# Optimization experiments

Measured on AMD Instinct MI355X. Metric: run time of the kernel, lower is better.

Reference implementation:

```python
import jax, jax.numpy as jnp
import numpy as np

EMB = 128   # embedding_dim
ND = 128    # node_dim
B = 64      # graphs in batch
NN = 500    # n_nodes per graph
N = B * NN  # total nodes = 32000
E = 256000  # edges per edge set
M = 20      # history length in input_


def _lin_params(key, out_dim, in_dim, bias=True):
    k1, k2 = jax.random.split(key)
    s = 1.0 / np.sqrt(in_dim)
    w = jax.random.uniform(k1, (out_dim, in_dim), jnp.float32, -s, s)
    if bias:
        b = jax.random.uniform(k2, (out_dim,), jnp.float32, -s, s)
        return w, b
    return w


def setup_inputs() -> dict:
    key = jax.random.key(0)
    ks = jax.random.split(key, 40)
    inp = {}
    inp["state_"] = jax.random.normal(ks[0], (B, ND), jnp.float32)
    inp["input_"] = jax.random.normal(ks[1], (B, M, EMB), jnp.float32)
    inp["x"] = jax.random.normal(ks[2], (N, EMB), jnp.float32)
    inp["e_n"] = jax.random.randint(ks[3], (2, E), 0, N)
    inp["e_r0"] = jax.random.randint(ks[4], (2, E), 0, N)
    inp["e_r1"] = jax.random.randint(ks[5], (2, E), 0, N)
    inp["n_nodes"] = NN
    # GRU-like params
    inp["win"] = _lin_params(ks[6], ND, EMB, bias=False)
    inp["wz"], inp["bz"] = _lin_params(ks[7], ND, 2 * ND)
    inp["wr"], inp["br"] = _lin_params(ks[8], ND, 2 * ND)
    inp["wh"], inp["bh"] = _lin_params(ks[9], ND, 2 * ND)
    # GAT params: lin (out,in)+bias, attn (out, 2*out)+bias
    inp["g0_lw"], inp["g0_lb"] = _lin_params(ks[10], ND, EMB)
    inp["g0_aw"], inp["g0_ab"] = _lin_params(ks[11], ND, 2 * ND)
    inp["g1_lw"], inp["g1_lb"] = _lin_params(ks[12], ND, ND)
    inp["g1_aw"], inp["g1_ab"] = _lin_params(ks[13], ND, 2 * ND)
    inp["g2_lw"], inp["g2_lb"] = _lin_params(ks[14], ND, ND)
    inp["g2_aw"], inp["g2_ab"] = _lin_params(ks[15], ND, 2 * ND)
    inp["gn_lw"], inp["gn_lb"] = _lin_params(ks[16], ND, ND)
    inp["gn_aw"], inp["gn_ab"] = _lin_params(ks[17], ND, 2 * ND)
    # heads
    inp["pw"], inp["pb"] = _lin_params(ks[18], 1, ND)
    inp["mw"], inp["mb"] = _lin_params(ks[19], 1, ND)
    inp["sw"], inp["sb"] = _lin_params(ks[20], 1, ND)
    return inp


def gat_conv(x, ei, lw, lb, aw, ab, slope=0.2):
    """PyG GATConv variant: lin -> per-edge attn(cat(x_i,x_j)) -> leaky_relu ->
    per-dst segment softmax (per channel) -> scatter-add of x_j*alpha."""
    n = x.shape[0]
    sl = jnp.arange(n)
    src = jnp.concatenate([ei[0], sl])   # j (source)
    dst = jnp.concatenate([ei[1], sl])   # i (target; softmax + aggregation index)
    h = x @ lw.T + lb                    # [N, ND]
    hi = h[dst]                          # x_i  [E', ND]
    hj = h[src]                          # x_j  [E', ND]
    a = jnp.concatenate([hi, hj], axis=-1) @ aw.T + ab
    a = jax.nn.leaky_relu(a, slope)
    amax = jax.ops.segment_max(a, dst, num_segments=n)
    e = jnp.exp(a - amax[dst])
    denom = jax.ops.segment_sum(e, dst, num_segments=n)
    alpha = e / (denom[dst] + 1e-16)
    return jax.ops.segment_sum(hj * alpha, dst, num_segments=n)


def reference(state_, input_, x, e_n, e_r0, e_r1, n_nodes,
              win, wz, bz, wr, br, wh, bh,
              g0_lw, g0_lb, g0_aw, g0_ab,
              g1_lw, g1_lb, g1_aw, g1_ab,
              g2_lw, g2_lb, g2_aw, g2_ab,
              gn_lw, gn_lb, gn_aw, gn_ab,
              pw, pb, mw, mb, sw, sb):
    # GRU-like gated state update
    st = state_.reshape(-1, ND)
    inp = input_.reshape(st.shape[0], -1, EMB)
    i = jnp.mean(inp @ win.T, axis=1)              # [B, ND]
    si = jnp.concatenate([st, i], axis=-1)
    z = jax.nn.sigmoid(si @ wz.T + bz)
    r = jax.nn.sigmoid(si @ wr.T + br)
    hc = jnp.tanh(jnp.concatenate([r * st, i], axis=-1) @ wh.T + bh)
    h = (1 - z) * st + z * hc                      # [B, ND]

    # Stacked GAT layers
    g0 = gat_conv(x, e_n, g0_lw, g0_lb, g0_aw, g0_ab)
    g1 = gat_conv(g0, e_r1, g1_lw, g1_lb, g1_aw, g1_ab)
    g2 = gat_conv(g1, e_r1, g1_lw, g1_lb, g1_aw, g1_ab)
    g3 = gat_conv(g2, e_n, gn_lw, gn_lb, gn_aw, gn_ab) + g0
    g4 = gat_conv(g3, e_r0, g2_lw, g2_lb, g2_aw, g2_ab)
    g5 = gat_conv(g4, e_r0, g2_lw, g2_lb, g2_aw, g2_ab)
    gx = gat_conv(g5, e_n, gn_lw, gn_lb, gn_aw, gn_ab) + g3

    xg = gx.reshape(-1, n_nodes, ND)               # [B, NN, ND]
    xt = xg[:, 1:]                                 # skip depot node
    scores = (xt @ pw.T + pb)[..., 0]              # [B, NN-1]
    probs = jax.nn.softmax(scores, axis=-1)        # Categorical params
    a = jax.nn.elu((xt @ mw.T + mb)[..., 0]) + 2   # Beta alpha
    b = jax.nn.elu(jnp.abs((xt @ sw.T + sb)[..., 0])) + 2  # Beta beta
    return (h, probs, a, b)
```

## Files before the change

### kernel.cpp

```cpp
#include <hip/hip_runtime.h>
#include <hip/hip_bf16.h>

#define ND 128
#define EMB 128
#define BATCH 64
#define MM 20
#define NN 500
#define RPAD 8

typedef short bf16x8 __attribute__((ext_vector_type(8)));
typedef float f32x4 __attribute__((ext_vector_type(4)));

__device__ __forceinline__ float bf2f(unsigned short u) {
    union { unsigned int i; float f; } x; x.i = ((unsigned int)u) << 16; return x.f;
}
__device__ __forceinline__ unsigned short f2bf(float f) {
    union { float f; unsigned int i; } x; x.f = f;
    unsigned int r = x.i + 0x7fffu + ((x.i >> 16) & 1u);
    return (unsigned short)(r >> 16);
}
__device__ __forceinline__ float2 bfpair(unsigned int p) {
    union { unsigned int i; float f; } a, b;
    a.i = p << 16; b.i = p & 0xffff0000u;
    return make_float2(a.f, b.f);
}

struct EdgePtrs { const int* e[3]; };

__global__ void edge_hist3(EdgePtrs ep, int* __restrict__ cnt, int E, int N) {
    int li = blockIdx.y;
    const int* dst = ep.e[li] + E;
    int e = blockIdx.x * blockDim.x + threadIdx.x;
    if (e < E) atomicAdd(&cnt[(size_t)li * N + dst[e]], 1);
}

__global__ void exscan3(const int* __restrict__ cnt, int* __restrict__ rowptr, int n) {
    __shared__ int wsum[16];
    __shared__ int woff[16];
    int li = blockIdx.x;
    const int4* c4 = (const int4*)(cnt + (size_t)li * n);
    int* rp = rowptr + (size_t)li * (n + RPAD);
    int t = threadIdx.x;
    int lane = t & 63, wid = t >> 6;
    int n4 = n >> 2;

    int4 v[8];
    int s = 0;
#pragma unroll
    for (int i = 0; i < 8; ++i) {
        int idx = t * 8 + i;
        if (idx < n4) v[i] = c4[idx];
        else { v[i].x = v[i].y = v[i].z = v[i].w = 0; }
    }
#pragma unroll
    for (int i = 0; i < 8; ++i) s += v[i].x + v[i].y + v[i].z + v[i].w;

    int ps = s;
#pragma unroll
    for (int d = 1; d < 64; d <<= 1) {
        int u = __shfl_up(ps, d, 64);
        if (lane >= d) ps += u;
    }
    if (lane == 63) wsum[wid] = ps;
    __syncthreads();
    if (t == 0) {
        int r = 0;
        for (int i = 0; i < 16; ++i) { woff[i] = r; r += wsum[i]; }
    }
    __syncthreads();
    int run = woff[wid] + ps - s;
    int4* rp4 = (int4*)rp;
#pragma unroll
    for (int i = 0; i < 8; ++i) {
        int idx = t * 8 + i;
        if (idx < n4) {
            int4 o;
            o.x = run; run += v[i].x;
            o.y = run; run += v[i].y;
            o.z = run; run += v[i].z;
            o.w = run; run += v[i].w;
            rp4[idx] = o;
        }
    }
    if (t == (n - 1) / 32) rp[n] = run;
}

__global__ void edge_scatter3(EdgePtrs ep, const int* __restrict__ rowptr, int* __restrict__ cnt,
                              int* __restrict__ col, int E, int N) {
    int li = blockIdx.y;
    const int* src = ep.e[li];
    const int* dst = src + E;
    const int* rp = rowptr + (size_t)li * (N + RPAD);
    int e = blockIdx.x * blockDim.x + threadIdx.x;
    if (e < E) {
        int d = dst[e];
        int p = atomicSub(&cnt[(size_t)li * N + d], 1) - 1;
        col[(size_t)li * E + rp[d] + p] = src[e];
    }
}

struct WcPtrs {
    const float* lw[4]; const float* lb[4]; const float* aw[4]; const float* ab[4];
    unsigned short* Whi[4]; unsigned short* Wlo[4]; float* Bf[4];
};

__global__ void make_wc4(WcPtrs p) {
    int set = blockIdx.y;
    const float* lw = p.lw[set]; const float* lb = p.lb[set];
    const float* aw = p.aw[set]; const float* ab = p.ab[set];
    int n = blockIdx.x;
    int e = threadIdx.x;
    float w;
    if (n < 128) {
        w = lw[n * 128 + e];
    } else if (n < 256) {
        int ni = n - 128; float s = 0.f;
        for (int k = 0; k < 128; ++k) s += aw[ni * 256 + k] * lw[k * 128 + e];
        w = s;
    } else {
        int nj = n - 256; float s = 0.f;
        for (int k = 0; k < 128; ++k) s += aw[nj * 256 + 128 + k] * lw[k * 128 + e];
        w = s;
    }
    unsigned short hi = f2bf(w);
    p.Whi[set][n * 128 + e] = hi;
    p.Wlo[set][n * 128 + e] = f2bf(w - bf2f(hi));
    if (e == 0) {
        float b;
        if (n < 128) b = lb[n];
        else if (n < 256) {
            int ni = n - 128; float s = ab[ni];
            for (int k = 0; k < 128; ++k) s += aw[ni * 256 + k] * lb[k];
            b = s;
        } else {
            int nj = n - 256; float s = 0.f;
            for (int k = 0; k < 128; ++k) s += aw[nj * 256 + 128 + k] * lb[k];
            b = s;
        }
        p.Bf[set][n] = b;
    }
}

__launch_bounds__(384)
__global__ void lin_fused(const float* __restrict__ X,
                          const unsigned short* __restrict__ Whi,
                          const unsigned short* __restrict__ Wlo,
                          const float* __restrict__ bias,
                          void* __restrict__ hu, int M) {
    const int slab = threadIdx.x >> 6;
    const int lane = threadIdx.x & 63;
    const int r16 = lane & 15;
    const int quad = lane >> 4;

    unsigned short* hu16 = (unsigned short*)hu;
    float* huf = (float*)hu;

    const unsigned short* Wh = Whi + (size_t)slab * 64 * 128;
    const unsigned short* Wl = Wlo + (size_t)slab * 64 * 128;
    bf16x8 wh[4][4], wl[4][4];
#pragma unroll
    for (int nt = 0; nt < 4; ++nt)
#pragma unroll
        for (int ks = 0; ks < 4; ++ks) {
            wh[nt][ks] = *(const bf16x8*)(Wh + (nt * 16 + r16) * 128 + ks * 32 + quad * 8);
            wl[nt][ks] = *(const bf16x8*)(Wl + (nt * 16 + r16) * 128 + ks * 32 + quad * 8);
        }
    float bv[4];
#pragma unroll
    for (int nt = 0; nt < 4; ++nt) bv[nt] = bias[slab * 64 + nt * 16 + r16];

    const int mt_count = M >> 4;
    for (int mt = blockIdx.x; mt < mt_count; mt += gridDim.x) {
        bf16x8 ah[4], al[4];
#pragma unroll
        for (int ks = 0; ks < 4; ++ks) {
            const float* xp = X + (size_t)(mt * 16 + r16) * 128 + ks * 32 + quad * 8;
            float4 v0 = *(const float4*)xp;
            float4 v1 = *(const float4*)(xp + 4);
            float v[8] = {v0.x, v0.y, v0.z, v0.w, v1.x, v1.y, v1.z, v1.w};
#pragma unroll
            for (int j = 0; j < 8; ++j) {
                unsigned short h = f2bf(v[j]);
                ah[ks][j] = (short)h;
                al[ks][j] = (short)f2bf(v[j] - bf2f(h));
            }
        }
#pragma unroll
        for (int nt = 0; nt < 4; ++nt) {
            f32x4 acc = {bv[nt], bv[nt], bv[nt], bv[nt]};
#pragma unroll
            for (int ks = 0; ks < 4; ++ks) {
                acc = __builtin_amdgcn_mfma_f32_16x16x32_bf16(ah[ks], wh[nt][ks], acc, 0, 0, 0);
                acc = __builtin_amdgcn_mfma_f32_16x16x32_bf16(al[ks], wh[nt][ks], acc, 0, 0, 0);
                acc = __builtin_amdgcn_mfma_f32_16x16x32_bf16(ah[ks], wl[nt][ks], acc, 0, 0, 0);
            }
            int col = slab * 64 + nt * 16 + r16;
#pragma unroll
            for (int r = 0; r < 4; ++r) {
                size_t row = (size_t)(mt * 16 + quad * 4 + r);
                if (slab < 2) {
                    int c = col;
                    hu16[row * 512 + ((c & ~1) << 1) + (c & 1)] = f2bf(acc[r]);
                } else if (slab < 4) {
                    int c = col - 128;
                    huf[row * 256 + 128 + c] = acc[r];
                } else {
                    int c = col - 256;
                    hu16[row * 512 + ((c & ~1) << 1) + 2 + (c & 1)] = f2bf(acc[r]);
                }
            }
        }
    }
}

__global__ void gat_agg(const void* __restrict__ hu,
                        const int* __restrict__ rowptr, const int* __restrict__ col,
                        const float* __restrict__ resid,
                        float* __restrict__ out, int N) {
    int wid = (int)((blockIdx.x * blockDim.x + threadIdx.x) >> 6);
    if (wid >= N) return;
    int lane = threadIdx.x & 63;
    const uint2* P = (const uint2*)hu;
    const float2* U = (const float2*)hu;

    float2 uiv = U[(size_t)wid * 128 + 64 + lane];
    uint2 sp = P[(size_t)wid * 128 + lane];
    float2 hs = bfpair(sp.x);
    float2 ujs = bfpair(sp.y);

    float a0 = uiv.x + ujs.x; a0 = a0 > 0.f ? a0 : 0.2f * a0;
    float a1 = uiv.y + ujs.y; a1 = a1 > 0.f ? a1 : 0.2f * a1;
    float m0 = a0, m1 = a1, l0 = 1.f, l1 = 1.f;
    float acc0 = hs.x, acc1 = hs.y;

#define AGG_STEP(pk)                                                      \
    {                                                                     \
        float2 hj = bfpair(pk.x);                                         \
        float2 uj = bfpair(pk.y);                                         \
        float b0 = uiv.x + uj.x; b0 = b0 > 0.f ? b0 : 0.2f * b0;          \
        float b1 = uiv.y + uj.y; b1 = b1 > 0.f ? b1 : 0.2f * b1;          \
        float n0 = fmaxf(m0, b0), n1 = fmaxf(m1, b1);                     \
        float s0 = __expf(m0 - n0), s1 = __expf(m1 - n1);                 \
        float p0 = __expf(b0 - n0), p1 = __expf(b1 - n1);                 \
        l0 = l0 * s0 + p0;            l1 = l1 * s1 + p1;                  \
        acc0 = acc0 * s0 + hj.x * p0; acc1 = acc1 * s1 + hj.y * p1;       \
        m0 = n0; m1 = n1;                                                 \
    }

    int e = rowptr[wid], end = rowptr[wid + 1];
    for (; e + 8 <= end; e += 8) {
        int s0i = col[e],     s1i = col[e + 1], s2i = col[e + 2], s3i = col[e + 3];
        int s4i = col[e + 4], s5i = col[e + 5], s6i = col[e + 6], s7i = col[e + 7];
        uint2 p0 = P[(size_t)s0i * 128 + lane];
        uint2 p1 = P[(size_t)s1i * 128 + lane];
        uint2 p2 = P[(size_t)s2i * 128 + lane];
        uint2 p3 = P[(size_t)s3i * 128 + lane];
        uint2 p4 = P[(size_t)s4i * 128 + lane];
        uint2 p5 = P[(size_t)s5i * 128 + lane];
        uint2 p6 = P[(size_t)s6i * 128 + lane];
        uint2 p7 = P[(size_t)s7i * 128 + lane];
        AGG_STEP(p0);
        AGG_STEP(p1);
        AGG_STEP(p2);
        AGG_STEP(p3);
        AGG_STEP(p4);
        AGG_STEP(p5);
        AGG_STEP(p6);
        AGG_STEP(p7);
    }
    for (; e + 4 <= end; e += 4) {
        int sA = col[e], sB = col[e + 1], sC = col[e + 2], sD = col[e + 3];
        uint2 pA = P[(size_t)sA * 128 + lane];
        uint2 pB = P[(size_t)sB * 128 + lane];
        uint2 pC = P[(size_t)sC * 128 + lane];
        uint2 pD = P[(size_t)sD * 128 + lane];
        AGG_STEP(pA);
        AGG_STEP(pB);
        AGG_STEP(pC);
        AGG_STEP(pD);
    }
    for (; e < end; ++e) {
        int sA = col[e];
        uint2 pA = P[(size_t)sA * 128 + lane];
        AGG_STEP(pA);
    }
#undef AGG_STEP

    float o0 = acc0 / (l0 + 1e-16f);
    float o1 = acc1 / (l1 + 1e-16f);
    if (resid) {
        float2 rv = ((const float2*)resid)[(size_t)wid * 64 + lane];
        o0 += rv.x; o1 += rv.y;
    }
    ((float2*)out)[(size_t)wid * 64 + lane] = make_float2(o0, o1);
}

__global__ void gru_kernel(const float* __restrict__ st_, const float* __restrict__ in_,
                           const float* __restrict__ win,
                           const float* __restrict__ wz, const float* __restrict__ bz,
                           const float* __restrict__ wr, const float* __restrict__ br,
                           const float* __restrict__ wh, const float* __restrict__ bh,
                           float* __restrict__ out) {
    __shared__ float sst[ND], sib[EMB], si[ND], srs[ND];
    int b = blockIdx.x, d = threadIdx.x;
    float s = 0.f;
    for (int m = 0; m < MM; ++m) s += in_[((size_t)b * MM + m) * EMB + d];
    sib[d] = s * (1.0f / MM);
    sst[d] = st_[b * ND + d];
    __syncthreads();
    float iv = 0.f;
    for (int e = 0; e < EMB; ++e) iv += sib[e] * win[d * EMB + e];
    si[d] = iv;
    __syncthreads();
    float za = bz[d], ra = br[d];
    for (int e = 0; e < ND; ++e) {
        za += sst[e] * wz[d * 2 * ND + e] + si[e] * wz[d * 2 * ND + ND + e];
        ra += sst[e] * wr[d * 2 * ND + e] + si[e] * wr[d * 2 * ND + ND + e];
    }
    float z = 1.f / (1.f + __expf(-za));
    float r = 1.f / (1.f + __expf(-ra));
    srs[d] = r * sst[d];
    __syncthreads();
    float ha = bh[d];
    for (int e = 0; e < ND; ++e)
        ha += srs[e] * wh[d * 2 * ND + e] + si[e] * wh[d * 2 * ND + ND + e];
    float hc = tanhf(ha);
    out[b * ND + d] = (1.f - z) * sst[d] + z * hc;
}

__global__ void heads_dots(const float* __restrict__ gx,
                           const float* __restrict__ pw_,
                           const float* __restrict__ mw_, const float* __restrict__ mb_,
                           const float* __restrict__ sw_, const float* __restrict__ sbias_,
                           float* __restrict__ scores, float* __restrict__ out) {
    int t = blockIdx.x;
    int lane = threadIdx.x & 63;
    int b = blockIdx.y * 4 + (threadIdx.x >> 6);
    const float2* g2 = (const float2*)gx;
    float2 pwv = ((const float2*)pw_)[lane];
    float2 mwv = ((const float2*)mw_)[lane];
    float2 swv = ((const float2*)sw_)[lane];
    int node = b * NN + 1 + t;
    float2 xv = g2[(size_t)node * 64 + lane];
    float dp = xv.x * pwv.x + xv.y * pwv.y;
    float dm = xv.x * mwv.x + xv.y * mwv.y;
    float ds = xv.x * swv.x + xv.y * swv.y;
    for (int off = 32; off; off >>= 1) {
        dp += __shfl_xor(dp, off);
        dm += __shfl_xor(dm, off);
        ds += __shfl_xor(ds, off);
    }
    if (lane == 0) {
        scores[(size_t)b * (NN - 1) + t] = dp;
        float av = dm + mb_[0]; av = av > 0.f ? av : (__expf(av) - 1.f);
        float bv = fabsf(ds + sbias_[0]);
        float* oA = out + BATCH * ND + (size_t)BATCH * (NN - 1);
        float* oB = oA + (size_t)BATCH * (NN - 1);
        oA[(size_t)b * (NN - 1) + t] = av + 2.f;
        oB[(size_t)b * (NN - 1) + t] = bv + 2.f;
    }
}

__global__ void heads_softmax(const float* __restrict__ scores, float* __restrict__ out) {
    __shared__ float scs[NN - 1], red[256];
    int b = blockIdx.x, tid = threadIdx.x;
    float mx = -1e30f;
    for (int t = tid; t < NN - 1; t += 256) { float v = scores[(size_t)b * (NN - 1) + t]; scs[t] = v; mx = fmaxf(mx, v); }
    red[tid] = mx; __syncthreads();
    for (int off = 128; off; off >>= 1) { if (tid < off) red[tid] = fmaxf(red[tid], red[tid + off]); __syncthreads(); }
    mx = red[0]; __syncthreads();
    float sum = 0.f;
    for (int t = tid; t < NN - 1; t += 256) { float e = __expf(scs[t] - mx); scs[t] = e; sum += e; }
    red[tid] = sum; __syncthreads();
    for (int off = 128; off; off >>= 1) { if (tid < off) red[tid] += red[tid + off]; __syncthreads(); }
    float inv = 1.0f / red[0];
    float* oP = out + BATCH * ND + (size_t)b * (NN - 1);
    for (int t = tid; t < NN - 1; t += 256) oP[t] = scs[t] * inv;
}

extern "C" void kernel_launch(void* const* d_in, const int* in_sizes, int n_in,
                              void* d_out, int out_size, void* d_ws, size_t ws_size,
                              hipStream_t stream) {
    const float* state_ = (const float*)d_in[0];
    const float* input_ = (const float*)d_in[1];
    const float* x      = (const float*)d_in[2];
    const int* e_n  = (const int*)d_in[3];
    const int* e_r0 = (const int*)d_in[4];
    const int* e_r1 = (const int*)d_in[5];
    const float* win = (const float*)d_in[7];
    const float* wz  = (const float*)d_in[8];
    const float* bz  = (const float*)d_in[9];
    const float* wr  = (const float*)d_in[10];
    const float* br  = (const float*)d_in[11];
    const float* wh  = (const float*)d_in[12];
    const float* bh  = (const float*)d_in[13];
    const float* pw = (const float*)d_in[30];
    const float* mw = (const float*)d_in[32];
    const float* mb = (const float*)d_in[33];
    const float* sw = (const float*)d_in[34];
    const float* sb = (const float*)d_in[35];
    float* out = (float*)d_out;

    const int E = in_sizes[3] / 2;
    const int N = in_sizes[2] / EMB;

    char* w = (char*)d_ws;
    auto alloc = [&](size_t bytes) { char* p = w; w += (bytes + 255) & ~(size_t)255; return p; };
    int* rpbase = (int*)alloc(3 * (size_t)(N + RPAD) * sizeof(int));
    int* colbase = (int*)alloc(3 * (size_t)E * sizeof(int));
    int* tmp = (int*)alloc(3 * (size_t)N * sizeof(int));
    unsigned short* Whi[4]; unsigned short* Wlo[4]; float* Bf[4];
    for (int i = 0; i < 4; ++i) {
        Whi[i] = (unsigned short*)alloc(384 * 128 * 2);
        Wlo[i] = (unsigned short*)alloc(384 * 128 * 2);
        Bf[i]  = (float*)alloc(384 * 4);
    }
    void* hu = (void*)alloc((size_t)N * 1024);
    float* ga = (float*)alloc((size_t)N * 128 * 4);
    float* gb = (float*)alloc((size_t)N * 128 * 4);
    float* gc = (float*)alloc((size_t)N * 128 * 4);
    float* scores = (float*)alloc((size_t)BATCH * (NN - 1) * 4);

    EdgePtrs ep; ep.e[0] = e_n; ep.e[1] = e_r0; ep.e[2] = e_r1;

    hipMemsetAsync(tmp, 0, 3 * (size_t)N * sizeof(int), stream);
    edge_hist3<<<dim3((E + 255) / 256, 3), 256, 0, stream>>>(ep, tmp, E, N);
    exscan3<<<3, 1024, 0, stream>>>(tmp, rpbase, N);
    edge_scatter3<<<dim3((E + 255) / 256, 3), 256, 0, stream>>>(ep, rpbase, tmp, colbase, E, N);

    WcPtrs wp;
    wp.lw[0] = (const float*)d_in[14]; wp.lb[0] = (const float*)d_in[15];
    wp.aw[0] = (const float*)d_in[16]; wp.ab[0] = (const float*)d_in[17];
    wp.lw[1] = (const float*)d_in[18]; wp.lb[1] = (const float*)d_in[19];
    wp.aw[1] = (const float*)d_in[20]; wp.ab[1] = (const float*)d_in[21];
    wp.lw[2] = (const float*)d_in[22]; wp.lb[2] = (const float*)d_in[23];
    wp.aw[2] = (const float*)d_in[24]; wp.ab[2] = (const float*)d_in[25];
    wp.lw[3] = (const float*)d_in[26]; wp.lb[3] = (const float*)d_in[27];
    wp.aw[3] = (const float*)d_in[28]; wp.ab[3] = (const float*)d_in[29];
    for (int i = 0; i < 4; ++i) { wp.Whi[i] = Whi[i]; wp.Wlo[i] = Wlo[i]; wp.Bf[i] = Bf[i]; }
    make_wc4<<<dim3(384, 4), 128, 0, stream>>>(wp);

    gru_kernel<<<BATCH, ND, 0, stream>>>(state_, input_, win, wz, bz, wr, br, wh, bh, out);

    auto conv = [&](const float* in, int csr_i, int wi, const float* resid, float* o) {
        lin_fused<<<256, 384, 0, stream>>>(in, Whi[wi], Wlo[wi], Bf[wi], hu, N);
        gat_agg<<<(N * 64) / 256, 256, 0, stream>>>(hu, rpbase + (size_t)csr_i * (N + RPAD),
                                                    colbase + (size_t)csr_i * E, resid, o, N);
    };

    conv(x,  0, 0, nullptr, ga);
    conv(ga, 2, 1, nullptr, gb);
    conv(gb, 2, 1, nullptr, gc);
    conv(gc, 0, 3, ga,      gb);
    conv(gb, 1, 2, nullptr, gc);
    conv(gc, 1, 2, nullptr, ga);
    conv(ga, 0, 3, gb,      gc);

    heads_dots<<<dim3(NN - 1, 16), 256, 0, stream>>>(gc, pw, mw, mb, sw, sb, scores, out);
    heads_softmax<<<BATCH, 256, 0, stream>>>(scores, out);
}
```

Baseline: 653.3 us.

## Windowed CSR scatter with LDS-resident counters and row pointers

Replaces the per-edge global-atomic CSR scatter with a kernel in which each block owns a window of 4000 destination nodes. The block keeps that window's row pointers and counters in shared memory and scans the whole destination array, using LDS atomics only for edges that fall in its window. This removes contended global atomics and scattered row-pointer reads. The cost is that every block rereads all E destinations, and the grid is only 8x3 blocks of 1024 threads, which may leave most CUs idle.

```diff
diff --git a/kernel.cpp b/kernel.cpp
--- a/kernel.cpp
+++ b/kernel.cpp
@@ -7,6 +7,7 @@
 #define MM 20
 #define NN 500
 #define RPAD 8
+#define WNODES 4000
 
 typedef short bf16x8 __attribute__((ext_vector_type(8)));
 typedef float f32x4 __attribute__((ext_vector_type(4)));
@@ -85,17 +86,42 @@
     if (t == (n - 1) / 32) rp[n] = run;
 }
 
-__global__ void edge_scatter3(EdgePtrs ep, const int* __restrict__ rowptr, int* __restrict__ cnt,
-                              int* __restrict__ col, int E, int N) {
+__launch_bounds__(1024)
+__global__ void edge_scatter_win(EdgePtrs ep, const int* __restrict__ rowptr,
+                                 const int* __restrict__ cnt,
+                                 int* __restrict__ col, int E, int N) {
+    __shared__ int srp[WNODES];
+    __shared__ int scnt[WNODES];
     int li = blockIdx.y;
+    int w0 = blockIdx.x * WNODES;
+    int wn = min(WNODES, N - w0);
     const int* src = ep.e[li];
     const int* dst = src + E;
     const int* rp = rowptr + (size_t)li * (N + RPAD);
-    int e = blockIdx.x * blockDim.x + threadIdx.x;
-    if (e < E) {
-        int d = dst[e];
-        int p = atomicSub(&cnt[(size_t)li * N + d], 1) - 1;
-        col[(size_t)li * E + rp[d] + p] = src[e];
+    const int* cn = cnt + (size_t)li * N;
+    int* cl = col + (size_t)li * E;
+
+    for (int i = threadIdx.x; i < wn; i += 1024) {
+        srp[i] = rp[w0 + i];
+        scnt[i] = cn[w0 + i];
+    }
+    __syncthreads();
+
+    int t = threadIdx.x;
+    const int4* d4 = (const int4*)dst;
+    int e4 = E >> 2;
+    for (int i = t; i < e4; i += 1024) {
+        int4 d = d4[i];
+        int base = i * 4;
+        int dd;
+        dd = d.x - w0; if ((unsigned)dd < (unsigned)wn) { int p = atomicSub(&scnt[dd], 1) - 1; cl[srp[dd] + p] = src[base]; }
+        dd = d.y - w0; if ((unsigned)dd < (unsigned)wn) { int p = atomicSub(&scnt[dd], 1) - 1; cl[srp[dd] + p] = src[base + 1]; }
+        dd = d.z - w0; if ((unsigned)dd < (unsigned)wn) { int p = atomicSub(&scnt[dd], 1) - 1; cl[srp[dd] + p] = src[base + 2]; }
+        dd = d.w - w0; if ((unsigned)dd < (unsigned)wn) { int p = atomicSub(&scnt[dd], 1) - 1; cl[srp[dd] + p] = src[base + 3]; }
+    }
+    for (int e = e4 * 4 + t; e < E; e += 1024) {
+        int dd = dst[e] - w0;
+        if ((unsigned)dd < (unsigned)wn) { int p = atomicSub(&scnt[dd], 1) - 1; cl[srp[dd] + p] = src[e]; }
     }
 }
 
@@ -426,7 +452,7 @@
     hipMemsetAsync(tmp, 0, 3 * (size_t)N * sizeof(int), stream);
     edge_hist3<<<dim3((E + 255) / 256, 3), 256, 0, stream>>>(ep, tmp, E, N);
     exscan3<<<3, 1024, 0, stream>>>(tmp, rpbase, N);
-    edge_scatter3<<<dim3((E + 255) / 256, 3), 256, 0, stream>>>(ep, rpbase, tmp, colbase, E, N);
+    edge_scatter_win<<<dim3((N + WNODES - 1) / WNODES, 3), 1024, 0, stream>>>(ep, rpbase, tmp, colbase, E, N);
 
     WcPtrs wp;
     wp.lw[0] = (const float*)d_in[14]; wp.lb[0] = (const float*)d_in[15];
```

Result: slower. 708.1 us (+8.4%).
